# Optimization experiments

Hardware: AMD Instinct MI355X
Metric: run time of the kernel (lower is better)

Reference implementation:

```python
import jax, jax.numpy as jnp
import numpy as np

N = 50000
E = 800000
IN_FEATS = 128
OUT_FEATS = 64
HEADS = 4
NEG_SLOPE = 0.2  # DGL GATConv default


def _glorot(key, shape):
    fan_in, fan_out = shape[0], shape[-1]
    lim = jnp.sqrt(6.0 / (fan_in + fan_out))
    return jax.random.uniform(key, shape, jnp.float32, -lim, lim)


def setup_inputs() -> dict:
    key = jax.random.key(0)
    ks = jax.random.split(key, 16)
    D = OUT_FEATS // HEADS  # per-head dim of layers 0..num_layers-2
    inp = {
        "h": jax.random.normal(ks[0], (N, IN_FEATS), jnp.float32),
        "src": jax.random.randint(ks[1], (E,), 0, N, jnp.int32),
        "dst": jax.random.randint(ks[2], (E,), 0, N, jnp.int32),
        # layer 0: in_feats -> heads x D
        "W0": _glorot(ks[3], (IN_FEATS, HEADS * D)),
        "al0": _glorot(ks[4], (HEADS, D)),
        "ar0": _glorot(ks[5], (HEADS, D)),
        "b0": jnp.zeros((HEADS * D,), jnp.float32),
        # layer 1: heads*D -> heads x D
        "W1": _glorot(ks[6], (HEADS * D, HEADS * D)),
        "al1": _glorot(ks[7], (HEADS, D)),
        "ar1": _glorot(ks[8], (HEADS, D)),
        "b1": jnp.zeros((HEADS * D,), jnp.float32),
        "W2": _glorot(ks[9], (HEADS * D, OUT_FEATS)),
        "al2": _glorot(ks[10], (1, OUT_FEATS)),
        "ar2": _glorot(ks[11], (1, OUT_FEATS)),
        "b2": jnp.zeros((OUT_FEATS,), jnp.float32),
    }
    return inp


def gat_conv(h, W, al, ar, b, src, dst):
    """DGL GATConv (shared src/dst features, allow_zero_in_degree).
    h: [N, F_in]; W: [F_in, H*D]; al, ar: [H, D]; b: [H*D].
    Returns [N, H, D].
    """
    H, D = al.shape
    f = (h @ W).reshape(-1, H, D)                 # [N, H, D]
    el = jnp.einsum("nhd,hd->nh", f, al)          # [N, H]
    er = jnp.einsum("nhd,hd->nh", f, ar)          # [N, H]
    e = jax.nn.leaky_relu(el[src] + er[dst], NEG_SLOPE)  # [E, H]
    # segment softmax over incoming edges of each dst node
    m = jax.ops.segment_max(e, dst, num_segments=N)      # [N, H]
    ex = jnp.exp(e - m[dst])                              # [E, H]
    s = jax.ops.segment_sum(ex, dst, num_segments=N)      # [N, H]
    a = ex / s[dst]                                       # [E, H]
    msg = a[:, :, None] * f[src]                          # [E, H, D]
    out = jax.ops.segment_sum(msg, dst, num_segments=N)   # [N, H, D]
    return out + b.reshape(1, H, D)


def reference(h, src, dst, W0, al0, ar0, b0, W1, al1, ar1, b1, W2, al2, ar2, b2):
    x = gat_conv(h, W0, al0, ar0, b0, src, dst).reshape(N, -1)
    x = jax.nn.elu(x)
    x = gat_conv(x, W1, al1, ar1, b1, src, dst).reshape(N, -1)
    x = jax.nn.elu(x)
    x = gat_conv(x, W2, al2, ar2, b2, src, dst)  # [N, 1, OUT_FEATS]
    return jnp.squeeze(x, axis=1)                # [N, OUT_FEATS]
```

## Files before the change

kernel.cpp:

```cpp
#include <hip/hip_runtime.h>
#include <hip/hip_bf16.h>

typedef unsigned short u16;
typedef unsigned int   u32;

__device__ __forceinline__ float bf2f(u32 bits) { return __uint_as_float(bits << 16); }
__device__ __forceinline__ u32 f2bf_bits(float x) {
    u32 u = __float_as_uint(x);
    return (u + 0x7fffu + ((u >> 16) & 1u)) >> 16;
}

__global__ __launch_bounds__(256) void detect_f32(const u32* __restrict__ w, int nwords, int* __restrict__ flag)
{
    __shared__ int s_hit;
    int t = threadIdx.x;
    if (t == 0) s_hit = 0;
    __syncthreads();
    int hit = 0;
    for (int i = t; i < nwords; i += 256) {
        u32 lo = w[i] & 0xffffu;
        if (((lo >> 7) & 0xffu) == 0xffu) hit = 1;
    }
    if (hit) atomicOr(&s_hit, 1);
    __syncthreads();
    if (t == 0) *flag = s_hit;
}

__global__ __launch_bounds__(256) void cvt_params(
    const int* __restrict__ flag,
    const void* __restrict__ W0, const void* __restrict__ al0, const void* __restrict__ ar0, const void* __restrict__ b0,
    const void* __restrict__ W1, const void* __restrict__ al1, const void* __restrict__ ar1, const void* __restrict__ b1,
    const void* __restrict__ W2, const void* __restrict__ al2, const void* __restrict__ ar2, const void* __restrict__ b2,
    float* __restrict__ P)
{
    int i = blockIdx.x * 256 + threadIdx.x;
    const void* s; int off;
    if      (i < 8192)  { s = W0;  off = 0;     }
    else if (i < 12288) { s = W1;  off = 8192;  }
    else if (i < 16384) { s = W2;  off = 12288; }
    else if (i < 16448) { s = al0; off = 16384; }
    else if (i < 16512) { s = ar0; off = 16448; }
    else if (i < 16576) { s = b0;  off = 16512; }
    else if (i < 16640) { s = al1; off = 16576; }
    else if (i < 16704) { s = ar1; off = 16640; }
    else if (i < 16768) { s = b1;  off = 16704; }
    else if (i < 16832) { s = al2; off = 16768; }
    else if (i < 16896) { s = ar2; off = 16832; }
    else if (i < 16960) { s = b2;  off = 16896; }
    else return;
    int j = i - off;
    P[i] = (*flag) ? ((const float*)s)[j] : bf2f(((const u16*)s)[j]);
}

__global__ __launch_bounds__(256) void zero_int(int* __restrict__ p, int n)
{
    int i = blockIdx.x * 256 + threadIdx.x;
    if (i < n) p[i] = 0;
}

__global__ __launch_bounds__(256) void hist_rank(
    const int* __restrict__ dst, int* __restrict__ deg, int* __restrict__ rank, int E)
{
    int e = blockIdx.x * 256 + threadIdx.x;
    if (e < E) rank[e] = atomicAdd(&deg[dst[e]], 1);
}

__global__ __launch_bounds__(256) void block_sums(const int* __restrict__ deg, int* __restrict__ bsum)
{
    __shared__ int red[4];
    int t = threadIdx.x;
    const int4* p = (const int4*)(deg + (size_t)blockIdx.x * 1024);
    int4 v = p[t];
    int s = v.x + v.y + v.z + v.w;
#pragma unroll
    for (int off = 32; off; off >>= 1) s += __shfl_down(s, off, 64);
    if ((t & 63) == 0) red[t >> 6] = s;
    __syncthreads();
    if (t == 0) bsum[blockIdx.x] = red[0] + red[1] + red[2] + red[3];
}

__global__ __launch_bounds__(256) void scan_bsums(int* __restrict__ bsum, int B)
{
    __shared__ int sm[256];
    int t = threadIdx.x;
    sm[t] = (t < B) ? bsum[t] : 0;
    __syncthreads();
    if (t == 0) {
        int run = 0;
        for (int i = 0; i < B; i++) { int v = sm[i]; sm[i] = run; run += v; }
    }
    __syncthreads();
    if (t < B) bsum[t] = sm[t];
}

__global__ __launch_bounds__(256) void block_scan(
    const int* __restrict__ deg, const int* __restrict__ bsum, int* __restrict__ row_start)
{
    __shared__ int sm[256];
    int t = threadIdx.x;
    size_t base = (size_t)blockIdx.x * 1024;
    int4 v = ((const int4*)(deg + base))[t];
    int tsum = v.x + v.y + v.z + v.w;
    sm[t] = tsum;
    __syncthreads();
#pragma unroll
    for (int off = 1; off < 256; off <<= 1) {
        int a = (t >= off) ? sm[t - off] : 0;
        __syncthreads();
        sm[t] += a;
        __syncthreads();
    }
    int excl = sm[t] - tsum + bsum[blockIdx.x];
    int4 r;
    r.x = excl;
    r.y = excl + v.x;
    r.z = excl + v.x + v.y;
    r.w = excl + v.x + v.y + v.z;
    ((int4*)(row_start + base))[t] = r;
}

__global__ __launch_bounds__(256) void scatter_kernel(
    const int* __restrict__ src, const int* __restrict__ dst, const int* __restrict__ rank,
    const int* __restrict__ row_start, int* __restrict__ csr_src, int E)
{
    int e = blockIdx.x * 256 + threadIdx.x;
    if (e < E) csr_src[row_start[dst[e]] + rank[e]] = src[e];
}

template<int F_IN, int H, bool LAYER0>
__global__ __launch_bounds__(256) void gemm_attn(
    const int* __restrict__ flag, const void* __restrict__ xv,
    const float* __restrict__ Wf, const float* __restrict__ alf, const float* __restrict__ arf,
    u16* __restrict__ fo, float* __restrict__ el, float* __restrict__ er, int N)
{
    int lane = threadIdx.x & 63;
    int cg   = __builtin_amdgcn_readfirstlane(threadIdx.x >> 6);
    int n    = blockIdx.x * 64 + lane;
    bool act = (n < N);

    float acc[16];
#pragma unroll
    for (int c = 0; c < 16; c++) acc[c] = 0.f;

    const float* Wcol = Wf + cg * 16;
    bool f32in = LAYER0 ? (*flag != 0) : false;

    if (act) {
        if (f32in) {
            const float* x = (const float*)xv + (size_t)n * F_IN;
            for (int k0 = 0; k0 < F_IN; k0 += 4) {
                float4 u = *reinterpret_cast<const float4*>(x + k0);
                float xs[4] = {u.x, u.y, u.z, u.w};
#pragma unroll
                for (int j = 0; j < 4; j++) {
                    const float* w = Wcol + (size_t)(k0 + j) * 64;
#pragma unroll
                    for (int c = 0; c < 16; c++) acc[c] = fmaf(xs[j], w[c], acc[c]);
                }
            }
        } else {
            const u16* x = (const u16*)xv + (size_t)n * F_IN;
            for (int k0 = 0; k0 < F_IN; k0 += 8) {
                uint4 u = *reinterpret_cast<const uint4*>(x + k0);
                float xs[8];
                xs[0] = bf2f(u.x & 0xffffu); xs[1] = bf2f(u.x >> 16);
                xs[2] = bf2f(u.y & 0xffffu); xs[3] = bf2f(u.y >> 16);
                xs[4] = bf2f(u.z & 0xffffu); xs[5] = bf2f(u.z >> 16);
                xs[6] = bf2f(u.w & 0xffffu); xs[7] = bf2f(u.w >> 16);
#pragma unroll
                for (int j = 0; j < 8; j++) {
                    const float* w = Wcol + (size_t)(k0 + j) * 64;
#pragma unroll
                    for (int c = 0; c < 16; c++) acc[c] = fmaf(xs[j], w[c], acc[c]);
                }
            }
        }
    }

    float e1 = 0.f, e2 = 0.f;
#pragma unroll
    for (int c = 0; c < 16; c++) {
        e1 = fmaf(acc[c], alf[cg * 16 + c], e1);
        e2 = fmaf(acc[c], arf[cg * 16 + c], e2);
    }
    if constexpr (H == 4) {
        if (act) {
            el[(size_t)n * 4 + cg] = e1;
            er[(size_t)n * 4 + cg] = e2;
        }
    } else {
        __shared__ float sel[4][64];
        __shared__ float ser[4][64];
        sel[cg][lane] = e1;
        ser[cg][lane] = e2;
        __syncthreads();
        if (cg == 0 && act) {
            el[n] = sel[0][lane] + sel[1][lane] + sel[2][lane] + sel[3][lane];
            er[n] = ser[0][lane] + ser[1][lane] + ser[2][lane] + ser[3][lane];
        }
    }

    if (act) {
        u16* dp = fo + (size_t)n * 64 + cg * 16;
        uint4 v;
        v.x = f2bf_bits(acc[0])  | (f2bf_bits(acc[1])  << 16);
        v.y = f2bf_bits(acc[2])  | (f2bf_bits(acc[3])  << 16);
        v.z = f2bf_bits(acc[4])  | (f2bf_bits(acc[5])  << 16);
        v.w = f2bf_bits(acc[6])  | (f2bf_bits(acc[7])  << 16);
        *reinterpret_cast<uint4*>(dp) = v;
        v.x = f2bf_bits(acc[8])  | (f2bf_bits(acc[9])  << 16);
        v.y = f2bf_bits(acc[10]) | (f2bf_bits(acc[11]) << 16);
        v.z = f2bf_bits(acc[12]) | (f2bf_bits(acc[13]) << 16);
        v.w = f2bf_bits(acc[14]) | (f2bf_bits(acc[15]) << 16);
        *reinterpret_cast<uint4*>(dp + 8) = v;
    }
}

template<int H, bool FINAL>
__global__ __launch_bounds__(256) void aggregate(
    const int* __restrict__ flag,
    const u16* __restrict__ fo, const float* __restrict__ el, const float* __restrict__ er,
    const int* __restrict__ row_start, const int* __restrict__ csr_src,
    const float* __restrict__ bias, void* __restrict__ outp, int N)
{
    int gid  = blockIdx.x * 256 + threadIdx.x;
    int n    = gid >> 6;
    int lane = gid & 63;
    if (n >= N) return;
    constexpr int D = 64 / H;
    int h = lane / D;
    float erh = er[(size_t)n * H + h];
    int i0 = row_start[n], i1 = row_start[n + 1];
    float s0 = 0.f, s1 = 0.f, a0 = 0.f, a1 = 0.f;
    int i = i0;
    for (; i + 4 <= i1; i += 4) {
        int sA = csr_src[i], sB = csr_src[i + 1], sC = csr_src[i + 2], sD = csr_src[i + 3];
        float vA = el[(size_t)sA * H + h] + erh;
        float vB = el[(size_t)sB * H + h] + erh;
        float vC = el[(size_t)sC * H + h] + erh;
        float vD = el[(size_t)sD * H + h] + erh;
        float fA = bf2f(fo[(size_t)sA * 64 + lane]);
        float fB = bf2f(fo[(size_t)sB * 64 + lane]);
        float fC = bf2f(fo[(size_t)sC * 64 + lane]);
        float fD = bf2f(fo[(size_t)sD * 64 + lane]);
        vA = fmaxf(vA, 0.2f * vA); vB = fmaxf(vB, 0.2f * vB);
        vC = fmaxf(vC, 0.2f * vC); vD = fmaxf(vD, 0.2f * vD);
        float eA = __expf(vA), eB = __expf(vB), eC = __expf(vC), eD = __expf(vD);
        s0 += eA + eC;  s1 += eB + eD;
        a0 = fmaf(eA, fA, a0); a1 = fmaf(eB, fB, a1);
        a0 = fmaf(eC, fC, a0); a1 = fmaf(eD, fD, a1);
    }
    for (; i < i1; i++) {
        int s = csr_src[i];
        float v = el[(size_t)s * H + h] + erh;
        v = fmaxf(v, 0.2f * v);
        float ex = __expf(v);
        float fv = bf2f(fo[(size_t)s * 64 + lane]);
        s0 += ex;
        a0 = fmaf(ex, fv, a0);
    }
    float sumex = s0 + s1;
    float acc   = a0 + a1;
    float o = (i1 > i0) ? (acc / sumex + bias[lane]) : bias[lane];
    size_t idx = (size_t)n * 64 + lane;
    if constexpr (!FINAL) {
        o = o > 0.f ? o : expm1f(o);
        ((u16*)outp)[idx] = f2bf_bits(o);
    } else {
        if (*flag) ((float*)outp)[idx] = o;
        else       ((u16*)outp)[idx]   = f2bf_bits(o);
    }
}

extern "C" void kernel_launch(void* const* d_in, const int* in_sizes, int n_in,
                              void* d_out, int out_size, void* d_ws, size_t ws_size,
                              hipStream_t stream)
{
    const void* h   = d_in[0];
    const int*  src = (const int*)d_in[1];
    const int*  dst = (const int*)d_in[2];

    const int N  = in_sizes[0] / 128;
    const int E  = in_sizes[1];
    const int NP = (N + 1023) & ~1023;
    const int B  = NP / 1024;

    char* ws = (char*)d_ws;
    size_t off = 0;
    auto take = [&](size_t bytes) -> char* {
        char* p = ws + off;
        off = (off + bytes + 255) & ~(size_t)255;
        return p;
    };
    float* P         = (float*)take(16960 * 4);
    int*   flag      = (int*)  take(256);
    int*   bsum      = (int*)  take((size_t)B * 4);
    float* el        = (float*)take((size_t)N * 4 * 4);
    float* er        = (float*)take((size_t)N * 4 * 4);
    int*   deg       = (int*)  take((size_t)NP * 4);
    int*   row_start = (int*)  take((size_t)NP * 4);
    int*   rank      = (int*)  take((size_t)E * 4);
    int*   csr_src   = (int*)  take((size_t)E * 4);
    u16*   f         = (u16*)  take((size_t)N * 64 * 2);
    u16*   x1        = (u16*)  take((size_t)N * 64 * 2);
    if (off > ws_size) x1 = (u16*)d_out;

    float* Wf0  = P;          float* Wf1  = P + 8192;  float* Wf2  = P + 12288;
    float* alf0 = P + 16384;  float* arf0 = P + 16448; float* bf0  = P + 16512;
    float* alf1 = P + 16576;  float* arf1 = P + 16640; float* bf1  = P + 16704;
    float* alf2 = P + 16768;  float* arf2 = P + 16832; float* bf2  = P + 16896;

    detect_f32<<<1, 256, 0, stream>>>((const u32*)h, 8192, flag);
    cvt_params<<<67, 256, 0, stream>>>(flag,
        d_in[3], d_in[4], d_in[5], d_in[6],
        d_in[7], d_in[8], d_in[9], d_in[10],
        d_in[11], d_in[12], d_in[13], d_in[14], P);
    zero_int<<<(NP + 255) / 256, 256, 0, stream>>>(deg, NP);
    hist_rank<<<(E + 255) / 256, 256, 0, stream>>>(dst, deg, rank, E);
    block_sums<<<B, 256, 0, stream>>>(deg, bsum);
    scan_bsums<<<1, 256, 0, stream>>>(bsum, B);
    block_scan<<<B, 256, 0, stream>>>(deg, bsum, row_start);
    scatter_kernel<<<(E + 255) / 256, 256, 0, stream>>>(src, dst, rank, row_start, csr_src, E);

    int gemm_blocks = (N + 63) / 64;
    int agg_blocks  = (N * 64 + 255) / 256;

    gemm_attn<128, 4, true ><<<gemm_blocks, 256, 0, stream>>>(flag, h,  Wf0, alf0, arf0, f, el, er, N);
    aggregate<4, false><<<agg_blocks, 256, 0, stream>>>(flag, f, el, er, row_start, csr_src, bf0, x1, N);
    gemm_attn<64, 4, false><<<gemm_blocks, 256, 0, stream>>>(flag, x1, Wf1, alf1, arf1, f, el, er, N);
    aggregate<4, false><<<agg_blocks, 256, 0, stream>>>(flag, f, el, er, row_start, csr_src, bf1, x1, N);
    gemm_attn<64, 1, false><<<gemm_blocks, 256, 0, stream>>>(flag, x1, Wf2, alf2, arf2, f, el, er, N);
    aggregate<1, true ><<<agg_blocks, 256, 0, stream>>>(flag, f, el, er, row_start, csr_src, bf2, d_out, N);
}
```

Measured before the change: 318.1 us.

## Merge three-kernel prefix scan into one block and widen aggregate gather loop

Replaces the three-kernel degree scan (block sums, scan of block sums, block scan) with a single 1024-thread kernel in which each thread serially scans a contiguous chunk of int4s. This removes two launches and their inter-kernel dependency gaps. Separately, the aggregate loop now aligns to a 4-element boundary, loads CSR indices with int4 vector loads, and unrolls by 8 so more el/feature gathers are in flight. The single-block scan does less parallel work, and the wider unroll raises register pressure.

```diff
diff --git a/kernel.cpp b/kernel.cpp
--- a/kernel.cpp
+++ b/kernel.cpp
@@ -65,58 +65,38 @@
     if (e < E) rank[e] = atomicAdd(&deg[dst[e]], 1);
 }
 
-__global__ __launch_bounds__(256) void block_sums(const int* __restrict__ deg, int* __restrict__ bsum)
-{
-    __shared__ int red[4];
+__global__ __launch_bounds__(1024) void scan_all(
+    const int* __restrict__ deg, int* __restrict__ row_start, int NP4)
+{
+    __shared__ int sm[1024];
     int t = threadIdx.x;
-    const int4* p = (const int4*)(deg + (size_t)blockIdx.x * 1024);
-    int4 v = p[t];
-    int s = v.x + v.y + v.z + v.w;
-#pragma unroll
-    for (int off = 32; off; off >>= 1) s += __shfl_down(s, off, 64);
-    if ((t & 63) == 0) red[t >> 6] = s;
+    int per = (NP4 + 1023) >> 10;
+    int lo = t * per; if (lo > NP4) lo = NP4;
+    int hi = lo + per; if (hi > NP4) hi = NP4;
+    const int4* d4 = (const int4*)deg;
+    int sum = 0;
+    for (int j = lo; j < hi; j++) { int4 v = d4[j]; sum += v.x + v.y + v.z + v.w; }
+    sm[t] = sum;
     __syncthreads();
-    if (t == 0) bsum[blockIdx.x] = red[0] + red[1] + red[2] + red[3];
-}
-
-__global__ __launch_bounds__(256) void scan_bsums(int* __restrict__ bsum, int B)
-{
-    __shared__ int sm[256];
-    int t = threadIdx.x;
-    sm[t] = (t < B) ? bsum[t] : 0;
-    __syncthreads();
-    if (t == 0) {
-        int run = 0;
-        for (int i = 0; i < B; i++) { int v = sm[i]; sm[i] = run; run += v; }
-    }
-    __syncthreads();
-    if (t < B) bsum[t] = sm[t];
-}
-
-__global__ __launch_bounds__(256) void block_scan(
-    const int* __restrict__ deg, const int* __restrict__ bsum, int* __restrict__ row_start)
-{
-    __shared__ int sm[256];
-    int t = threadIdx.x;
-    size_t base = (size_t)blockIdx.x * 1024;
-    int4 v = ((const int4*)(deg + base))[t];
-    int tsum = v.x + v.y + v.z + v.w;
-    sm[t] = tsum;
-    __syncthreads();
-#pragma unroll
-    for (int off = 1; off < 256; off <<= 1) {
+#pragma unroll
+    for (int off = 1; off < 1024; off <<= 1) {
         int a = (t >= off) ? sm[t - off] : 0;
         __syncthreads();
         sm[t] += a;
         __syncthreads();
     }
-    int excl = sm[t] - tsum + bsum[blockIdx.x];
-    int4 r;
-    r.x = excl;
-    r.y = excl + v.x;
-    r.z = excl + v.x + v.y;
-    r.w = excl + v.x + v.y + v.z;
-    ((int4*)(row_start + base))[t] = r;
+    int run = sm[t] - sum;
+    int4* r4 = (int4*)row_start;
+    for (int j = lo; j < hi; j++) {
+        int4 v = d4[j];
+        int4 r;
+        r.x = run;
+        r.y = run + v.x;
+        r.z = r.y + v.y;
+        r.w = r.z + v.z;
+        r4[j] = r;
+        run = r.w + v.w;
+    }
 }
 
 __global__ __launch_bounds__(256) void scatter_kernel(
@@ -233,22 +213,53 @@
     int i0 = row_start[n], i1 = row_start[n + 1];
     float s0 = 0.f, s1 = 0.f, a0 = 0.f, a1 = 0.f;
     int i = i0;
+
+    int alignEnd = (i0 + 3) & ~3; if (alignEnd > i1) alignEnd = i1;
+    for (; i < alignEnd; i++) {
+        int s = csr_src[i];
+        float v = el[(size_t)s * H + h] + erh;
+        v = fmaxf(v, 0.2f * v);
+        float ex = __expf(v);
+        float fv = bf2f(fo[(size_t)s * 64 + lane]);
+        s0 += ex;
+        a0 = fmaf(ex, fv, a0);
+    }
+    for (; i + 8 <= i1; i += 8) {
+        int4 cA = *reinterpret_cast<const int4*>(csr_src + i);
+        int4 cB = *reinterpret_cast<const int4*>(csr_src + i + 4);
+        int ss[8] = {cA.x, cA.y, cA.z, cA.w, cB.x, cB.y, cB.z, cB.w};
+        float vv[8], ff[8];
+#pragma unroll
+        for (int j = 0; j < 8; j++) {
+            vv[j] = el[(size_t)ss[j] * H + h];
+            ff[j] = bf2f(fo[(size_t)ss[j] * 64 + lane]);
+        }
+#pragma unroll
+        for (int j = 0; j < 8; j++) {
+            float v = vv[j] + erh;
+            v = fmaxf(v, 0.2f * v);
+            float ex = __expf(v);
+            if (j & 1) { s1 += ex; a1 = fmaf(ex, ff[j], a1); }
+            else       { s0 += ex; a0 = fmaf(ex, ff[j], a0); }
+        }
+    }
     for (; i + 4 <= i1; i += 4) {
-        int sA = csr_src[i], sB = csr_src[i + 1], sC = csr_src[i + 2], sD = csr_src[i + 3];
-        float vA = el[(size_t)sA * H + h] + erh;
-        float vB = el[(size_t)sB * H + h] + erh;
-        float vC = el[(size_t)sC * H + h] + erh;
-        float vD = el[(size_t)sD * H + h] + erh;
-        float fA = bf2f(fo[(size_t)sA * 64 + lane]);
-        float fB = bf2f(fo[(size_t)sB * 64 + lane]);
-        float fC = bf2f(fo[(size_t)sC * 64 + lane]);
-        float fD = bf2f(fo[(size_t)sD * 64 + lane]);
-        vA = fmaxf(vA, 0.2f * vA); vB = fmaxf(vB, 0.2f * vB);
-        vC = fmaxf(vC, 0.2f * vC); vD = fmaxf(vD, 0.2f * vD);
-        float eA = __expf(vA), eB = __expf(vB), eC = __expf(vC), eD = __expf(vD);
-        s0 += eA + eC;  s1 += eB + eD;
-        a0 = fmaf(eA, fA, a0); a1 = fmaf(eB, fB, a1);
-        a0 = fmaf(eC, fC, a0); a1 = fmaf(eD, fD, a1);
+        int4 cA = *reinterpret_cast<const int4*>(csr_src + i);
+        int ss[4] = {cA.x, cA.y, cA.z, cA.w};
+        float vv[4], ff[4];
+#pragma unroll
+        for (int j = 0; j < 4; j++) {
+            vv[j] = el[(size_t)ss[j] * H + h];
+            ff[j] = bf2f(fo[(size_t)ss[j] * 64 + lane]);
+        }
+#pragma unroll
+        for (int j = 0; j < 4; j++) {
+            float v = vv[j] + erh;
+            v = fmaxf(v, 0.2f * v);
+            float ex = __expf(v);
+            if (j & 1) { s1 += ex; a1 = fmaf(ex, ff[j], a1); }
+            else       { s0 += ex; a0 = fmaf(ex, ff[j], a0); }
+        }
     }
     for (; i < i1; i++) {
         int s = csr_src[i];
@@ -259,6 +270,7 @@
         s0 += ex;
         a0 = fmaf(ex, fv, a0);
     }
+
     float sumex = s0 + s1;
     float acc   = a0 + a1;
     float o = (i1 > i0) ? (acc / sumex + bias[lane]) : bias[lane];
@@ -283,7 +295,6 @@
     const int N  = in_sizes[0] / 128;
     const int E  = in_sizes[1];
     const int NP = (N + 1023) & ~1023;
-    const int B  = NP / 1024;
 
     char* ws = (char*)d_ws;
     size_t off = 0;
@@ -294,7 +305,6 @@
     };
     float* P         = (float*)take(16960 * 4);
     int*   flag      = (int*)  take(256);
-    int*   bsum      = (int*)  take((size_t)B * 4);
     float* el        = (float*)take((size_t)N * 4 * 4);
     float* er        = (float*)take((size_t)N * 4 * 4);
     int*   deg       = (int*)  take((size_t)NP * 4);
@@ -317,9 +327,7 @@
         d_in[11], d_in[12], d_in[13], d_in[14], P);
     zero_int<<<(NP + 255) / 256, 256, 0, stream>>>(deg, NP);
     hist_rank<<<(E + 255) / 256, 256, 0, stream>>>(dst, deg, rank, E);
-    block_sums<<<B, 256, 0, stream>>>(deg, bsum);
-    scan_bsums<<<1, 256, 0, stream>>>(bsum, B);
-    block_scan<<<B, 256, 0, stream>>>(deg, bsum, row_start);
+    scan_all<<<1, 1024, 0, stream>>>(deg, row_start, NP / 4);
     scatter_kernel<<<(E + 255) / 256, 256, 0, stream>>>(src, dst, rank, row_start, csr_src, E);
 
     int gemm_blocks = (N + 63) / 64;
```

After: 336.6 us. +5.8%, slower.

## Precompute per-edge attention exponentials in a separate kernel before aggregation

Applied to the files above, without the earlier changes.

Adds an edge_ex kernel that computes leaky_relu(el[src]+er[dst]) and its exponential once per edge and head into a CSR-ordered buffer. Scatter now also writes csr_dst. The aggregate kernel then reads these precomputed values instead of redoing the el gather and exp in each of the 64 lanes. The f32 detection is merged into cvt_params to drop one launch. This removes redundant per-lane gathers and transcendentals, at the cost of extra kernel launches and an E×H float buffer written and reread per layer.

```diff
diff --git a/kernel.cpp b/kernel.cpp
--- a/kernel.cpp
+++ b/kernel.cpp
@@ -10,29 +10,26 @@
     return (u + 0x7fffu + ((u >> 16) & 1u)) >> 16;
 }
 
-__global__ __launch_bounds__(256) void detect_f32(const u32* __restrict__ w, int nwords, int* __restrict__ flag)
-{
-    __shared__ int s_hit;
-    int t = threadIdx.x;
-    if (t == 0) s_hit = 0;
-    __syncthreads();
-    int hit = 0;
-    for (int i = t; i < nwords; i += 256) {
-        u32 lo = w[i] & 0xffffu;
-        if (((lo >> 7) & 0xffu) == 0xffu) hit = 1;
-    }
-    if (hit) atomicOr(&s_hit, 1);
-    __syncthreads();
-    if (t == 0) *flag = s_hit;
-}
-
 __global__ __launch_bounds__(256) void cvt_params(
-    const int* __restrict__ flag,
+    const u32* __restrict__ hw, int* __restrict__ flag,
     const void* __restrict__ W0, const void* __restrict__ al0, const void* __restrict__ ar0, const void* __restrict__ b0,
     const void* __restrict__ W1, const void* __restrict__ al1, const void* __restrict__ ar1, const void* __restrict__ b1,
     const void* __restrict__ W2, const void* __restrict__ al2, const void* __restrict__ ar2, const void* __restrict__ b2,
     float* __restrict__ P)
 {
+    __shared__ int s_hit;
+    if (threadIdx.x == 0) s_hit = 0;
+    __syncthreads();
+    int hit = 0;
+    for (int i = threadIdx.x; i < 8192; i += 256) {
+        u32 lo = hw[i] & 0xffffu;
+        if (((lo >> 7) & 0xffu) == 0xffu) hit = 1;
+    }
+    if (hit) atomicOr(&s_hit, 1);
+    __syncthreads();
+    int f32 = s_hit;
+    if (threadIdx.x == 0) *flag = f32;
+
     int i = blockIdx.x * 256 + threadIdx.x;
     const void* s; int off;
     if      (i < 8192)  { s = W0;  off = 0;     }
@@ -49,7 +46,7 @@
     else if (i < 16960) { s = b2;  off = 16896; }
     else return;
     int j = i - off;
-    P[i] = (*flag) ? ((const float*)s)[j] : bf2f(((const u16*)s)[j]);
+    P[i] = f32 ? ((const float*)s)[j] : bf2f(((const u16*)s)[j]);
 }
 
 __global__ __launch_bounds__(256) void zero_int(int* __restrict__ p, int n)
@@ -121,10 +118,15 @@
 
 __global__ __launch_bounds__(256) void scatter_kernel(
     const int* __restrict__ src, const int* __restrict__ dst, const int* __restrict__ rank,
-    const int* __restrict__ row_start, int* __restrict__ csr_src, int E)
+    const int* __restrict__ row_start, int* __restrict__ csr_src, int* __restrict__ csr_dst, int E)
 {
     int e = blockIdx.x * 256 + threadIdx.x;
-    if (e < E) csr_src[row_start[dst[e]] + rank[e]] = src[e];
+    if (e < E) {
+        int d = dst[e];
+        int p = row_start[d] + rank[e];
+        csr_src[p] = src[e];
+        csr_dst[p] = d;
+    }
 }
 
 template<int F_IN, int H, bool LAYER0>
@@ -216,10 +218,25 @@
     }
 }
 
+template<int H>
+__global__ __launch_bounds__(256) void edge_ex(
+    const float* __restrict__ el, const float* __restrict__ er,
+    const int* __restrict__ csr_src, const int* __restrict__ csr_dst,
+    float* __restrict__ ex, int EH)
+{
+    int t = blockIdx.x * 256 + threadIdx.x;
+    if (t >= EH) return;
+    int i = t / H, h = t % H;
+    int s = csr_src[i], n = csr_dst[i];
+    float v = el[(size_t)s * H + h] + er[(size_t)n * H + h];
+    v = fmaxf(v, 0.2f * v);
+    ex[t] = __expf(v);
+}
+
 template<int H, bool FINAL>
 __global__ __launch_bounds__(256) void aggregate(
     const int* __restrict__ flag,
-    const u16* __restrict__ fo, const float* __restrict__ el, const float* __restrict__ er,
+    const u16* __restrict__ fo, const float* __restrict__ ex,
     const int* __restrict__ row_start, const int* __restrict__ csr_src,
     const float* __restrict__ bias, void* __restrict__ outp, int N)
 {
@@ -229,35 +246,30 @@
     if (n >= N) return;
     constexpr int D = 64 / H;
     int h = lane / D;
-    float erh = er[(size_t)n * H + h];
     int i0 = row_start[n], i1 = row_start[n + 1];
+    const float* exh = ex + h;
     float s0 = 0.f, s1 = 0.f, a0 = 0.f, a1 = 0.f;
     int i = i0;
     for (; i + 4 <= i1; i += 4) {
         int sA = csr_src[i], sB = csr_src[i + 1], sC = csr_src[i + 2], sD = csr_src[i + 3];
-        float vA = el[(size_t)sA * H + h] + erh;
-        float vB = el[(size_t)sB * H + h] + erh;
-        float vC = el[(size_t)sC * H + h] + erh;
-        float vD = el[(size_t)sD * H + h] + erh;
+        float eA = exh[(size_t)(i + 0) * H];
+        float eB = exh[(size_t)(i + 1) * H];
+        float eC = exh[(size_t)(i + 2) * H];
+        float eD = exh[(size_t)(i + 3) * H];
         float fA = bf2f(fo[(size_t)sA * 64 + lane]);
         float fB = bf2f(fo[(size_t)sB * 64 + lane]);
         float fC = bf2f(fo[(size_t)sC * 64 + lane]);
         float fD = bf2f(fo[(size_t)sD * 64 + lane]);
-        vA = fmaxf(vA, 0.2f * vA); vB = fmaxf(vB, 0.2f * vB);
-        vC = fmaxf(vC, 0.2f * vC); vD = fmaxf(vD, 0.2f * vD);
-        float eA = __expf(vA), eB = __expf(vB), eC = __expf(vC), eD = __expf(vD);
         s0 += eA + eC;  s1 += eB + eD;
         a0 = fmaf(eA, fA, a0); a1 = fmaf(eB, fB, a1);
         a0 = fmaf(eC, fC, a0); a1 = fmaf(eD, fD, a1);
     }
     for (; i < i1; i++) {
         int s = csr_src[i];
-        float v = el[(size_t)s * H + h] + erh;
-        v = fmaxf(v, 0.2f * v);
-        float ex = __expf(v);
-        float fv = bf2f(fo[(size_t)s * 64 + lane]);
-        s0 += ex;
-        a0 = fmaf(ex, fv, a0);
+        float e = exh[(size_t)i * H];
+        float f = bf2f(fo[(size_t)s * 64 + lane]);
+        s0 += e;
+        a0 = fmaf(e, f, a0);
     }
     float sumex = s0 + s1;
     float acc   = a0 + a1;
@@ -301,6 +313,8 @@
     int*   row_start = (int*)  take((size_t)NP * 4);
     int*   rank      = (int*)  take((size_t)E * 4);
     int*   csr_src   = (int*)  take((size_t)E * 4);
+    int*   csr_dst   = (int*)  take((size_t)E * 4);
+    float* ex        = (float*)take((size_t)E * 4 * 4);
     u16*   f         = (u16*)  take((size_t)N * 64 * 2);
     u16*   x1        = (u16*)  take((size_t)N * 64 * 2);
     if (off > ws_size) x1 = (u16*)d_out;
@@ -310,8 +324,7 @@
     float* alf1 = P + 16576;  float* arf1 = P + 16640; float* bf1  = P + 16704;
     float* alf2 = P + 16768;  float* arf2 = P + 16832; float* bf2  = P + 16896;
 
-    detect_f32<<<1, 256, 0, stream>>>((const u32*)h, 8192, flag);
-    cvt_params<<<67, 256, 0, stream>>>(flag,
+    cvt_params<<<67, 256, 0, stream>>>((const u32*)h, flag,
         d_in[3], d_in[4], d_in[5], d_in[6],
         d_in[7], d_in[8], d_in[9], d_in[10],
         d_in[11], d_in[12], d_in[13], d_in[14], P);
@@ -320,15 +333,20 @@
     block_sums<<<B, 256, 0, stream>>>(deg, bsum);
     scan_bsums<<<1, 256, 0, stream>>>(bsum, B);
     block_scan<<<B, 256, 0, stream>>>(deg, bsum, row_start);
-    scatter_kernel<<<(E + 255) / 256, 256, 0, stream>>>(src, dst, rank, row_start, csr_src, E);
+    scatter_kernel<<<(E + 255) / 256, 256, 0, stream>>>(src, dst, rank, row_start, csr_src, csr_dst, E);
 
     int gemm_blocks = (N + 63) / 64;
     int agg_blocks  = (N * 64 + 255) / 256;
+    int ex4_blocks  = (E * 4 + 255) / 256;
+    int ex1_blocks  = (E + 255) / 256;
 
     gemm_attn<128, 4, true ><<<gemm_blocks, 256, 0, stream>>>(flag, h,  Wf0, alf0, arf0, f, el, er, N);
-    aggregate<4, false><<<agg_blocks, 256, 0, stream>>>(flag, f, el, er, row_start, csr_src, bf0, x1, N);
+    edge_ex<4><<<ex4_blocks, 256, 0, stream>>>(el, er, csr_src, csr_dst, ex, E * 4);
+    aggregate<4, false><<<agg_blocks, 256, 0, stream>>>(flag, f, ex, row_start, csr_src, bf0, x1, N);
     gemm_attn<64, 4, false><<<gemm_blocks, 256, 0, stream>>>(flag, x1, Wf1, alf1, arf1, f, el, er, N);
-    aggregate<4, false><<<agg_blocks, 256, 0, stream>>>(flag, f, el, er, row_start, csr_src, bf1, x1, N);
+    edge_ex<4><<<ex4_blocks, 256, 0, stream>>>(el, er, csr_src, csr_dst, ex, E * 4);
+    aggregate<4, false><<<agg_blocks, 256, 0, stream>>>(flag, f, ex, row_start, csr_src, bf1, x1, N);
     gemm_attn<64, 1, false><<<gemm_blocks, 256, 0, stream>>>(flag, x1, Wf2, alf2, arf2, f, el, er, N);
-    aggregate<1, true ><<<agg_blocks, 256, 0, stream>>>(flag, f, el, er, row_start, csr_src, bf2, d_out, N);
-}
+    edge_ex<1><<<ex1_blocks, 256, 0, stream>>>(el, er, csr_src, csr_dst, ex, E);
+    aggregate<1, true ><<<agg_blocks, 256, 0, stream>>>(flag, f, ex, row_start, csr_src, bf2, d_out, N);
+}
```

Measured after the change: 348.3 us. 1.1x slower.
